# Kernel tuning notes

Hardware: AMD Instinct MI355X
Metric: run time of the kernel (lower is better)

The kernel has to match this reference:

```python
import jax, jax.numpy as jnp
import numpy as np

SOS_TOKEN = 0
MAX_SEQ_LENGTH = 64
H = 1024   # hidden_size
V = 32000  # output_size (vocab)
B = 64     # batch


def setup_inputs() -> dict:
    key = jax.random.key(0)
    ks = jax.random.split(key, 10)
    s = 1.0 / np.sqrt(H)
    return {
        "encoder_outputs": jax.random.normal(ks[0], (B, 32, H), dtype=jnp.float32),
        "encoder_hidden": jax.random.normal(ks[1], (1, B, H), dtype=jnp.float32),
        "target_tensor": jax.random.randint(ks[2], (B, MAX_SEQ_LENGTH), 0, V),
        "emb": jax.random.normal(ks[3], (V, H), dtype=jnp.float32) * 0.02,
        "W_ih": jax.random.uniform(ks[4], (3 * H, H), minval=-s, maxval=s, dtype=jnp.float32),
        "W_hh": jax.random.uniform(ks[5], (3 * H, H), minval=-s, maxval=s, dtype=jnp.float32),
        "b_ih": jax.random.uniform(ks[6], (3 * H,), minval=-s, maxval=s, dtype=jnp.float32),
        "b_hh": jax.random.uniform(ks[7], (3 * H,), minval=-s, maxval=s, dtype=jnp.float32),
        "W_out": jax.random.uniform(ks[8], (V, H), minval=-s, maxval=s, dtype=jnp.float32),
        "b_out": jax.random.uniform(ks[9], (V,), minval=-s, maxval=s, dtype=jnp.float32),
    }


def reference(encoder_outputs, encoder_hidden, target_tensor,
              emb, W_ih, W_hh, b_ih, b_hh, W_out, b_out):
    # teacher forcing: input at step 0 is SOS, at step i>0 is target[:, i-1]
    bsz = encoder_outputs.shape[0]
    sos = jnp.full((bsz, 1), SOS_TOKEN, dtype=target_tensor.dtype)
    tokens = jnp.concatenate([sos, target_tensor[:, :MAX_SEQ_LENGTH - 1]], axis=1).T  # [T,B]
    h0 = encoder_hidden[0]  # num_layers=1 -> [B,H]

    def step(h, tok):
        x = jax.nn.relu(emb[tok])                       # [B,H] embed + relu
        gi = x @ W_ih.T + b_ih                          # [B,3H]
        gh = h @ W_hh.T + b_hh                          # [B,3H]
        ir, iz, inn = jnp.split(gi, 3, axis=-1)         # PyTorch gate order r,z,n
        hr, hz, hn = jnp.split(gh, 3, axis=-1)
        r = jax.nn.sigmoid(ir + hr)
        z = jax.nn.sigmoid(iz + hz)
        n = jnp.tanh(inn + r * hn)
        h_new = (1.0 - z) * n + z * h
        logits = h_new @ W_out.T + b_out                # [B,V]
        return h_new, logits

    h_final, logits = jax.lax.scan(step, h0, tokens)    # logits: [T,B,V]
    dec_out = jax.nn.log_softmax(jnp.transpose(logits, (1, 0, 2)), axis=-1)  # [B,T,V]
    return dec_out, h_final[None]  # hidden: [num_layers,B,H]
```

## Files before the change

### kernel.cpp

```cpp
#include <hip/hip_runtime.h>
#include <hip/hip_bf16.h>
#include <stdint.h>

#define H 1024
#define BATCH 64
#define TSTEPS 64
#define VOCAB 32000

typedef __attribute__((ext_vector_type(8))) short bf16x8;
typedef __attribute__((ext_vector_type(4))) float f32x4;

__device__ __forceinline__ uint16_t f2b(float f) {
  union { float f; uint32_t u; } v; v.f = f;
  uint32_t u = v.u;
  return (uint16_t)((u + 0x7FFFu + ((u >> 16) & 1u)) >> 16);
}

__device__ __forceinline__ void g2l16(const uint16_t* g, uint16_t* l) {
  __builtin_amdgcn_global_load_lds((const __attribute__((address_space(1))) void*)(g),
                                   (__attribute__((address_space(3))) void*)(l), 16, 0, 0);
}

__global__ void cast_bf16_kernel(const float* __restrict__ src, uint16_t* __restrict__ dst, int n4) {
  int i = blockIdx.x * blockDim.x + threadIdx.x;
  int stride = gridDim.x * blockDim.x;
  for (; i < n4; i += stride) {
    float4 f = ((const float4*)src)[i];
    union { uint16_t u[4]; uint64_t d; } o;
    o.u[0] = f2b(f.x); o.u[1] = f2b(f.y); o.u[2] = f2b(f.z); o.u[3] = f2b(f.w);
    ((uint64_t*)dst)[i] = o.d;
  }
}

__global__ void embed_kernel(const float* __restrict__ emb, const int* __restrict__ tgt,
                             uint16_t* __restrict__ X) {
  int i = blockIdx.x;
  int t = i >> 6, b = i & 63;
  int tok = (t == 0) ? 0 : tgt[b * TSTEPS + (t - 1)];
  const float4* src = (const float4*)(emb + (size_t)tok * H);
  uint64_t* dst = (uint64_t*)(X + (size_t)i * H);
  int k = threadIdx.x;
  float4 f = src[k];
  union { uint16_t u[4]; uint64_t d; } o;
  o.u[0] = f2b(fmaxf(f.x, 0.f)); o.u[1] = f2b(fmaxf(f.y, 0.f));
  o.u[2] = f2b(fmaxf(f.z, 0.f)); o.u[3] = f2b(fmaxf(f.w, 0.f));
  dst[k] = o.d;
}

__global__ void h0_kernel(const float* __restrict__ eh, uint16_t* __restrict__ hb0) {
  int i = blockIdx.x * blockDim.x + threadIdx.x;
  float4 f = ((const float4*)eh)[i];
  union { uint16_t u[4]; uint64_t d; } o;
  o.u[0] = f2b(f.x); o.u[1] = f2b(f.y); o.u[2] = f2b(f.z); o.u[3] = f2b(f.w);
  ((uint64_t*)hb0)[i] = o.d;
}

__global__ __launch_bounds__(256) void gi_gemm_kernel(
    const uint16_t* __restrict__ A,
    const uint16_t* __restrict__ Bm,
    const float* __restrict__ bias,
    float* __restrict__ out) {
  __shared__ uint16_t lA[128 * 32];
  __shared__ uint16_t lB[128 * 32];
  const int tid = threadIdx.x;
  const int lane = tid & 63;
  const int w = tid >> 6;
  const int wr = w >> 1, wc = w & 1;
  int flat = blockIdx.y * 24 + blockIdx.x;
  int nf = (flat & 7) * 96 + (flat >> 3);
  const int m0 = (nf / 24) * 128;
  const int n0 = (nf % 24) * 128;

  f32x4 acc[4][4];
#pragma unroll
  for (int mi = 0; mi < 4; ++mi)
#pragma unroll
    for (int ni = 0; ni < 4; ++ni) acc[mi][ni] = (f32x4){0, 0, 0, 0};

  const int srow = w * 16 + (lane >> 2);
  const int scol = (lane & 3) * 8;

  for (int k0 = 0; k0 < 1024; k0 += 32) {
    __syncthreads();
    g2l16(A + (size_t)(m0 + srow) * 1024 + k0 + scol,       &lA[w * 512]);
    g2l16(A + (size_t)(m0 + 64 + srow) * 1024 + k0 + scol,  &lA[2048 + w * 512]);
    g2l16(Bm + (size_t)(n0 + srow) * 1024 + k0 + scol,      &lB[w * 512]);
    g2l16(Bm + (size_t)(n0 + 64 + srow) * 1024 + k0 + scol, &lB[2048 + w * 512]);
    __syncthreads();
    bf16x8 a[4], b[4];
#pragma unroll
    for (int mi = 0; mi < 4; ++mi)
      a[mi] = *(const bf16x8*)&lA[(wr * 64 + mi * 16 + (lane & 15)) * 32 + (lane >> 4) * 8];
#pragma unroll
    for (int ni = 0; ni < 4; ++ni)
      b[ni] = *(const bf16x8*)&lB[(wc * 64 + ni * 16 + (lane & 15)) * 32 + (lane >> 4) * 8];
#pragma unroll
    for (int mi = 0; mi < 4; ++mi)
#pragma unroll
      for (int ni = 0; ni < 4; ++ni)
        acc[mi][ni] = __builtin_amdgcn_mfma_f32_16x16x32_bf16(a[mi], b[ni], acc[mi][ni], 0, 0, 0);
  }

#pragma unroll
  for (int ni = 0; ni < 4; ++ni) {
    int v = n0 + wc * 64 + ni * 16 + (lane & 15);
    float bv = bias[v];
#pragma unroll
    for (int mi = 0; mi < 4; ++mi) {
#pragma unroll
      for (int r = 0; r < 4; ++r) {
        int row = m0 + wr * 64 + mi * 16 + (lane >> 4) * 4 + r;
        out[(size_t)row * 3072 + v] = acc[mi][ni][r] + bv;
      }
    }
  }
}

__global__ __launch_bounds__(64) void step_kernel(
    const uint16_t* __restrict__ Whh_b,
    const float* __restrict__ gi,
    const float* __restrict__ b_hh,
    const float* __restrict__ h_cur,
    float* __restrict__ h_nxt,
    uint16_t* __restrict__ Hsb,
    int t) {
  const int lane = threadIdx.x;
  const int l15 = lane & 15, kq = lane >> 4;
  const int rg = blockIdx.x >> 6, cs = blockIdx.x & 63;
  const int m0 = rg * 16, c0 = cs * 16;
  const int c = c0 + l15;

  float gr[4], gz[4], gn[4], hold[4];
#pragma unroll
  for (int r = 0; r < 4; ++r) {
    int m = m0 + kq * 4 + r;
    const float* gp = gi + (size_t)(t * 64 + m) * 3072;
    gr[r] = gp[c]; gz[r] = gp[1024 + c]; gn[r] = gp[2048 + c];
    hold[r] = h_cur[(size_t)m * 1024 + c];
  }

  const uint16_t* ap = Hsb + (size_t)(t * 64 + m0 + l15) * 1024 + kq * 8;
  const uint16_t* br = Whh_b + (size_t)(c) * 1024 + kq * 8;
  const uint16_t* bz = Whh_b + (size_t)(1024 + c) * 1024 + kq * 8;
  const uint16_t* bn = Whh_b + (size_t)(2048 + c) * 1024 + kq * 8;

  f32x4 ar = {0,0,0,0}, az = {0,0,0,0}, an = {0,0,0,0};
#pragma unroll
  for (int kk = 0; kk < 32; ++kk) {
    bf16x8 a = *(const bf16x8*)(ap + kk * 32);
    ar = __builtin_amdgcn_mfma_f32_16x16x32_bf16(a, *(const bf16x8*)(br + kk * 32), ar, 0, 0, 0);
    az = __builtin_amdgcn_mfma_f32_16x16x32_bf16(a, *(const bf16x8*)(bz + kk * 32), az, 0, 0, 0);
    an = __builtin_amdgcn_mfma_f32_16x16x32_bf16(a, *(const bf16x8*)(bn + kk * 32), an, 0, 0, 0);
  }

  float bhr = b_hh[c], bhz = b_hh[1024 + c], bhn = b_hh[2048 + c];
#pragma unroll
  for (int r = 0; r < 4; ++r) {
    int m = m0 + kq * 4 + r;
    float rg_ = 1.f / (1.f + __expf(-(gr[r] + ar[r] + bhr)));
    float zg  = 1.f / (1.f + __expf(-(gz[r] + az[r] + bhz)));
    float ng  = tanhf(gn[r] + rg_ * (an[r] + bhn));
    float hnew = (1.f - zg) * ng + zg * hold[r];
    h_nxt[(size_t)m * 1024 + c] = hnew;
    Hsb[(size_t)((t + 1) * 64 + m) * 1024 + c] = f2b(hnew);
  }
}

__global__ __launch_bounds__(256) void out_gemm_kernel(
    const uint16_t* __restrict__ A,
    const uint16_t* __restrict__ Bm,
    const float* __restrict__ bias,
    float* __restrict__ out,
    float* __restrict__ px) {
  __shared__ uint16_t lA[128 * 32];
  __shared__ uint16_t lB[128 * 32];
  __shared__ float ssum[128][2];
  const int tid = threadIdx.x;
  const int lane = tid & 63;
  const int w = tid >> 6;
  const int wr = w >> 1, wc = w & 1;
  int flat = blockIdx.y * 250 + blockIdx.x;
  int xcd = flat & 7, i = flat >> 3;
  const int m0 = ((xcd << 2) | (i & 3)) * 128;
  const int n0 = (i >> 2) * 128;

  f32x4 acc[4][4];
#pragma unroll
  for (int mi = 0; mi < 4; ++mi)
#pragma unroll
    for (int ni = 0; ni < 4; ++ni) acc[mi][ni] = (f32x4){0, 0, 0, 0};

  const int srow = w * 16 + (lane >> 2);
  const int scol = (lane & 3) * 8;

  for (int k0 = 0; k0 < 1024; k0 += 32) {
    __syncthreads();
    g2l16(A + (size_t)(m0 + srow) * 1024 + k0 + scol,       &lA[w * 512]);
    g2l16(A + (size_t)(m0 + 64 + srow) * 1024 + k0 + scol,  &lA[2048 + w * 512]);
    g2l16(Bm + (size_t)(n0 + srow) * 1024 + k0 + scol,      &lB[w * 512]);
    g2l16(Bm + (size_t)(n0 + 64 + srow) * 1024 + k0 + scol, &lB[2048 + w * 512]);
    __syncthreads();
    bf16x8 a[4], b[4];
#pragma unroll
    for (int mi = 0; mi < 4; ++mi)
      a[mi] = *(const bf16x8*)&lA[(wr * 64 + mi * 16 + (lane & 15)) * 32 + (lane >> 4) * 8];
#pragma unroll
    for (int ni = 0; ni < 4; ++ni)
      b[ni] = *(const bf16x8*)&lB[(wc * 64 + ni * 16 + (lane & 15)) * 32 + (lane >> 4) * 8];
#pragma unroll
    for (int mi = 0; mi < 4; ++mi)
#pragma unroll
      for (int ni = 0; ni < 4; ++ni)
        acc[mi][ni] = __builtin_amdgcn_mfma_f32_16x16x32_bf16(a[mi], b[ni], acc[mi][ni], 0, 0, 0);
  }

  float rsum[4][4];
#pragma unroll
  for (int mi = 0; mi < 4; ++mi)
#pragma unroll
    for (int r = 0; r < 4; ++r) rsum[mi][r] = 0.f;

#pragma unroll
  for (int ni = 0; ni < 4; ++ni) {
    int v = n0 + wc * 64 + ni * 16 + (lane & 15);
    float bv = bias[v];
#pragma unroll
    for (int mi = 0; mi < 4; ++mi) {
#pragma unroll
      for (int r = 0; r < 4; ++r) {
        float x = acc[mi][ni][r] + bv;
        int row = m0 + wr * 64 + mi * 16 + (lane >> 4) * 4 + r;
        size_t off = (size_t)(row & 63) * (TSTEPS * (size_t)VOCAB)
                   + (size_t)(row >> 6) * VOCAB + v;
        __builtin_nontemporal_store(x, &out[off]);
        rsum[mi][r] += __expf(x);
      }
    }
  }
#pragma unroll
  for (int mask = 1; mask < 16; mask <<= 1)
#pragma unroll
    for (int mi = 0; mi < 4; ++mi)
#pragma unroll
      for (int r = 0; r < 4; ++r)
        rsum[mi][r] += __shfl_xor(rsum[mi][r], mask);

  if ((lane & 15) == 0) {
    int kq = lane >> 4;
#pragma unroll
    for (int mi = 0; mi < 4; ++mi)
#pragma unroll
      for (int r = 0; r < 4; ++r)
        ssum[wr * 64 + mi * 16 + kq * 4 + r][wc] = rsum[mi][r];
  }
  __syncthreads();
  if (tid < 128)
    px[(size_t)(m0 + tid) * 256 + (n0 >> 7)] = ssum[tid][0] + ssum[tid][1];
}

__global__ __launch_bounds__(256) void lsefin_kernel(
    const float* __restrict__ px, float* __restrict__ out) {
  const int tid = threadIdx.x;
  const int b = blockIdx.x >> 6, t = blockIdx.x & 63;
  const float* p = px + (size_t)(t * 64 + b) * 256;
  float s = (tid < 250) ? p[tid] : 0.f;
#pragma unroll
  for (int off = 1; off < 64; off <<= 1) s += __shfl_xor(s, off);
  __shared__ float ss[4];
  if ((tid & 63) == 0) ss[tid >> 6] = s;
  __syncthreads();
  float lse = logf(ss[0] + ss[1] + ss[2] + ss[3]);
  float* row = out + (size_t)blockIdx.x * VOCAB;
  for (int i = tid * 4; i < VOCAB; i += 1024) {
    f32x4 x = *(const f32x4*)(row + i);
    x[0] -= lse; x[1] -= lse; x[2] -= lse; x[3] -= lse;
    __builtin_nontemporal_store(x, (f32x4*)(row + i));
  }
}

__global__ void hcopy_kernel(const float* __restrict__ h, float* __restrict__ out) {
  int i = blockIdx.x * blockDim.x + threadIdx.x;
  ((float4*)out)[i] = ((const float4*)h)[i];
}

extern "C" void kernel_launch(void* const* d_in, const int* in_sizes, int n_in,
                              void* d_out, int out_size, void* d_ws, size_t ws_size,
                              hipStream_t stream) {
  const float* enc_hidden = (const float*)d_in[1];
  const int* tgt          = (const int*)d_in[2];
  const float* emb        = (const float*)d_in[3];
  const float* W_ih       = (const float*)d_in[4];
  const float* W_hh       = (const float*)d_in[5];
  const float* b_ih       = (const float*)d_in[6];
  const float* b_hh       = (const float*)d_in[7];
  const float* W_out      = (const float*)d_in[8];
  const float* b_out      = (const float*)d_in[9];
  float* out = (float*)d_out;

  char* ws = (char*)d_ws;
  float*    gi     = (float*)(ws);
  uint16_t* Wout_b = (uint16_t*)(ws);
  uint16_t* Wih_b  = (uint16_t*)(ws + 65536000);
  uint16_t* Whh_b  = (uint16_t*)(ws + 71827456);
  uint16_t* Xb     = (uint16_t*)(ws + 78118912);
  float*    px     = (float*)   (ws + 78118912);
  uint16_t* Hsb    = (uint16_t*)(ws + 86507520);
  float*    hA     = (float*)   (ws + 95027200);
  float*    hB     = (float*)   (ws + 95289344);

  cast_bf16_kernel<<<2048, 256, 0, stream>>>(W_ih, Wih_b, 3072 * 1024 / 4);
  cast_bf16_kernel<<<2048, 256, 0, stream>>>(W_hh, Whh_b, 3072 * 1024 / 4);
  embed_kernel<<<4096, 256, 0, stream>>>(emb, tgt, Xb);
  h0_kernel<<<64, 256, 0, stream>>>(enc_hidden, Hsb);

  dim3 gg(24, 32);
  gi_gemm_kernel<<<gg, 256, 0, stream>>>(Xb, Wih_b, b_ih, gi);

  for (int t = 0; t < TSTEPS; ++t) {
    const float* hc = (t == 0) ? enc_hidden : ((t & 1) ? hA : hB);
    float* hn       = (t & 1) ? hB : hA;
    step_kernel<<<256, 64, 0, stream>>>(Whh_b, gi, b_hh, hc, hn, Hsb, t);
  }

  cast_bf16_kernel<<<2048, 256, 0, stream>>>(W_out, Wout_b, VOCAB * 1024 / 4);

  dim3 g(250, 32);
  out_gemm_kernel<<<g, 256, 0, stream>>>(Hsb + 65536, Wout_b, b_out, out, px);
  lsefin_kernel<<<4096, 256, 0, stream>>>(px, out);
  hcopy_kernel<<<64, 256, 0, stream>>>((TSTEPS & 1) ? hB : hA, out + 131072000ull);
}
```

Measured before the change: 1.102 ms.

## Rewrite output GEMM as 256x256 tiled, double-buffered swizzled LDS pipeline; regroup step blocks

```diff
diff --git a/kernel.cpp b/kernel.cpp
--- a/kernel.cpp
+++ b/kernel.cpp
@@ -116,7 +116,7 @@
   }
 }
 
-__global__ __launch_bounds__(64) void step_kernel(
+__global__ __launch_bounds__(256) void step_kernel(
     const uint16_t* __restrict__ Whh_b,
     const float* __restrict__ gi,
     const float* __restrict__ b_hh,
@@ -124,10 +124,10 @@
     float* __restrict__ h_nxt,
     uint16_t* __restrict__ Hsb,
     int t) {
-  const int lane = threadIdx.x;
+  const int tid = threadIdx.x;
+  const int lane = tid & 63, w = tid >> 6;
   const int l15 = lane & 15, kq = lane >> 4;
-  const int rg = blockIdx.x >> 6, cs = blockIdx.x & 63;
-  const int m0 = rg * 16, c0 = cs * 16;
+  const int m0 = w * 16, c0 = blockIdx.x * 16;
   const int c = c0 + l15;
 
   float gr[4], gz[4], gn[4], hold[4];
@@ -166,70 +166,147 @@
   }
 }
 
-__global__ __launch_bounds__(256) void out_gemm_kernel(
-    const uint16_t* __restrict__ A,
-    const uint16_t* __restrict__ Bm,
+
+__device__ __forceinline__ void stageAH(const uint16_t* __restrict__ G, int grow0, int kt,
+                                        char* lbase, int w, int l) {
+#pragma unroll
+  for (int j = 0; j < 2; ++j) {
+    int c = w * 2 + j;
+    int r = c * 8 + (l >> 3);
+    int scol = ((l & 7) ^ (l >> 3)) * 8;
+    g2l16(G + (size_t)(grow0 + r) * 1024 + kt * 64 + scol, (uint16_t*)(lbase + c * 1024));
+  }
+}
+
+template<int D, int MP, bool RB>
+__device__ __forceinline__ void ph_read(const char* sm, int wr, int wc, int l15, int kq,
+                                        bf16x8 (&afr)[2][2], bf16x8 (&bfr)[4][2]) {
+#pragma unroll
+  for (int m = 0; m < 2; ++m) {
+    const int mi = MP * 2 + m;
+    const int h = mi >> 2;
+    const int r = wr * 64 + (mi & 3) * 16 + l15;
+    const char* base = sm + D * 65536 + h * 16384 + r * 128;
+#pragma unroll
+    for (int ks = 0; ks < 2; ++ks)
+      afr[m][ks] = *(const bf16x8*)(base + ((((ks << 2) + kq) ^ (r & 7)) << 4));
+  }
+  if constexpr (RB) {
+#pragma unroll
+    for (int ni = 0; ni < 4; ++ni) {
+      const int r = (wc & 1) * 64 + ni * 16 + l15;
+      const char* base = sm + D * 65536 + 32768 + (wc >> 1) * 16384 + r * 128;
+#pragma unroll
+      for (int ks = 0; ks < 2; ++ks)
+        bfr[ni][ks] = *(const bf16x8*)(base + ((((ks << 2) + kq) ^ (r & 7)) << 4));
+    }
+  }
+}
+
+template<int MP>
+__device__ __forceinline__ void ph_mma(f32x4 (&acc)[8][4], bf16x8 (&afr)[2][2], bf16x8 (&bfr)[4][2]) {
+  __builtin_amdgcn_s_setprio(1);
+#pragma unroll
+  for (int m = 0; m < 2; ++m)
+#pragma unroll
+    for (int ni = 0; ni < 4; ++ni)
+#pragma unroll
+      for (int ks = 0; ks < 2; ++ks)
+        acc[MP * 2 + m][ni] =
+            __builtin_amdgcn_mfma_f32_16x16x32_bf16(afr[m][ks], bfr[ni][ks], acc[MP * 2 + m][ni], 0, 0, 0);
+  __builtin_amdgcn_s_setprio(0);
+}
+
+#define PHX(D, MP, RB, STG, VM) { \
+  bf16x8 afr[2][2]; \
+  ph_read<D, MP, RB>(sm, wr, wc, l15, kq, afr, bfr); \
+  STG; \
+  __builtin_amdgcn_sched_barrier(0); \
+  if (VM == 1) asm volatile("s_waitcnt vmcnt(6)" ::: "memory"); \
+  if (VM == 2) asm volatile("s_waitcnt vmcnt(0)" ::: "memory"); \
+  __builtin_amdgcn_s_barrier(); \
+  ph_mma<MP>(acc, afr, bfr); \
+  __builtin_amdgcn_s_barrier(); \
+}
+
+__global__ __launch_bounds__(512, 1) void out_gemm_kernel(
+    const uint16_t* __restrict__ Ag,
+    const uint16_t* __restrict__ Bg,
     const float* __restrict__ bias,
     float* __restrict__ out,
     float* __restrict__ px) {
-  __shared__ uint16_t lA[128 * 32];
-  __shared__ uint16_t lB[128 * 32];
-  __shared__ float ssum[128][2];
+  extern __shared__ char sm[];
   const int tid = threadIdx.x;
-  const int lane = tid & 63;
-  const int w = tid >> 6;
-  const int wr = w >> 1, wc = w & 1;
+  const int l = tid & 63, w = tid >> 6;
+  const int l15 = l & 15, kq = l >> 4;
+  const int wr = w >> 2, wc = w & 3;
   int flat = blockIdx.y * 250 + blockIdx.x;
-  int xcd = flat & 7, i = flat >> 3;
-  const int m0 = ((xcd << 2) | (i & 3)) * 128;
-  const int n0 = (i >> 2) * 128;
-
-  f32x4 acc[4][4];
-#pragma unroll
-  for (int mi = 0; mi < 4; ++mi)
+  int xcd = flat & 7, i0 = flat >> 3;
+  const int m0 = ((xcd << 1) | (i0 & 1)) * 256;
+  const int n0 = (i0 >> 1) * 256;
+
+  char* const sA0 = sm;
+  char* const sA1 = sm + 16384;
+  char* const sB0 = sm + 32768;
+  char* const sB1 = sm + 49152;
+  char* const tA0 = sm + 65536;
+  char* const tA1 = sm + 81920;
+  char* const tB0 = sm + 98304;
+  char* const tB1 = sm + 114688;
+
+  f32x4 acc[8][4];
+#pragma unroll
+  for (int mi = 0; mi < 8; ++mi)
 #pragma unroll
     for (int ni = 0; ni < 4; ++ni) acc[mi][ni] = (f32x4){0, 0, 0, 0};
 
-  const int srow = w * 16 + (lane >> 2);
-  const int scol = (lane & 3) * 8;
-
-  for (int k0 = 0; k0 < 1024; k0 += 32) {
-    __syncthreads();
-    g2l16(A + (size_t)(m0 + srow) * 1024 + k0 + scol,       &lA[w * 512]);
-    g2l16(A + (size_t)(m0 + 64 + srow) * 1024 + k0 + scol,  &lA[2048 + w * 512]);
-    g2l16(Bm + (size_t)(n0 + srow) * 1024 + k0 + scol,      &lB[w * 512]);
-    g2l16(Bm + (size_t)(n0 + 64 + srow) * 1024 + k0 + scol, &lB[2048 + w * 512]);
-    __syncthreads();
-    bf16x8 a[4], b[4];
-#pragma unroll
-    for (int mi = 0; mi < 4; ++mi)
-      a[mi] = *(const bf16x8*)&lA[(wr * 64 + mi * 16 + (lane & 15)) * 32 + (lane >> 4) * 8];
-#pragma unroll
-    for (int ni = 0; ni < 4; ++ni)
-      b[ni] = *(const bf16x8*)&lB[(wc * 64 + ni * 16 + (lane & 15)) * 32 + (lane >> 4) * 8];
-#pragma unroll
-    for (int mi = 0; mi < 4; ++mi)
-#pragma unroll
-      for (int ni = 0; ni < 4; ++ni)
-        acc[mi][ni] = __builtin_amdgcn_mfma_f32_16x16x32_bf16(a[mi], b[ni], acc[mi][ni], 0, 0, 0);
-  }
-
-  float rsum[4][4];
-#pragma unroll
-  for (int mi = 0; mi < 4; ++mi)
+  stageAH(Bg, n0,       0, sB0, w, l);
+  stageAH(Bg, n0 + 128, 0, sB1, w, l);
+  stageAH(Ag, m0,       0, sA0, w, l);
+  stageAH(Ag, m0 + 128, 0, sA1, w, l);
+  stageAH(Bg, n0,       1, tB0, w, l);
+  stageAH(Bg, n0 + 128, 1, tB1, w, l);
+  stageAH(Ag, m0,       1, tA0, w, l);
+  asm volatile("s_waitcnt vmcnt(6)" ::: "memory");
+  __builtin_amdgcn_s_barrier();
+
+  bf16x8 bfr[4][2];
+  for (int i = 0; i < 7; ++i) {
+    PHX(0, 0, true,  stageAH(Ag, m0 + 128, 2 * i + 1, tA1, w, l), 0)
+    PHX(0, 1, false, stageAH(Bg, n0,       2 * i + 2, sB0, w, l), 0)
+    PHX(0, 2, false, stageAH(Bg, n0 + 128, 2 * i + 2, sB1, w, l), 0)
+    PHX(0, 3, false, stageAH(Ag, m0,       2 * i + 2, sA0, w, l), 1)
+    PHX(1, 0, true,  stageAH(Ag, m0 + 128, 2 * i + 2, sA1, w, l), 0)
+    PHX(1, 1, false, stageAH(Bg, n0,       2 * i + 3, tB0, w, l), 0)
+    PHX(1, 2, false, stageAH(Bg, n0 + 128, 2 * i + 3, tB1, w, l), 0)
+    PHX(1, 3, false, stageAH(Ag, m0,       2 * i + 3, tA0, w, l), 1)
+  }
+  PHX(0, 0, true,  stageAH(Ag, m0 + 128, 15, tA1, w, l), 0)
+  PHX(0, 1, false, , 0)
+  PHX(0, 2, false, , 0)
+  PHX(0, 3, false, , 2)
+  PHX(1, 0, true,  , 0)
+  PHX(1, 1, false, , 0)
+  PHX(1, 2, false, , 0)
+  PHX(1, 3, false, , 0)
+
+  float rsum[8][4];
+#pragma unroll
+  for (int mi = 0; mi < 8; ++mi)
 #pragma unroll
     for (int r = 0; r < 4; ++r) rsum[mi][r] = 0.f;
 
 #pragma unroll
   for (int ni = 0; ni < 4; ++ni) {
-    int v = n0 + wc * 64 + ni * 16 + (lane & 15);
+    int v = n0 + wc * 64 + ni * 16 + l15;
     float bv = bias[v];
 #pragma unroll
-    for (int mi = 0; mi < 4; ++mi) {
+    for (int mi = 0; mi < 8; ++mi) {
+      int tr = (mi < 4) ? (wr * 64 + mi * 16) : (128 + wr * 64 + (mi - 4) * 16);
 #pragma unroll
       for (int r = 0; r < 4; ++r) {
         float x = acc[mi][ni][r] + bv;
-        int row = m0 + wr * 64 + mi * 16 + (lane >> 4) * 4 + r;
+        int row = m0 + tr + kq * 4 + r;
         size_t off = (size_t)(row & 63) * (TSTEPS * (size_t)VOCAB)
                    + (size_t)(row >> 6) * VOCAB + v;
         __builtin_nontemporal_store(x, &out[off]);
@@ -240,30 +317,35 @@
 #pragma unroll
   for (int mask = 1; mask < 16; mask <<= 1)
 #pragma unroll
-    for (int mi = 0; mi < 4; ++mi)
+    for (int mi = 0; mi < 8; ++mi)
 #pragma unroll
       for (int r = 0; r < 4; ++r)
         rsum[mi][r] += __shfl_xor(rsum[mi][r], mask);
 
-  if ((lane & 15) == 0) {
-    int kq = lane >> 4;
-#pragma unroll
-    for (int mi = 0; mi < 4; ++mi)
+  __builtin_amdgcn_s_barrier();
+  float* ssum = (float*)sm;
+  if (l15 == 0) {
+#pragma unroll
+    for (int mi = 0; mi < 8; ++mi) {
+      int tr = (mi < 4) ? (wr * 64 + mi * 16) : (128 + wr * 64 + (mi - 4) * 16);
 #pragma unroll
       for (int r = 0; r < 4; ++r)
-        ssum[wr * 64 + mi * 16 + kq * 4 + r][wc] = rsum[mi][r];
-  }
-  __syncthreads();
-  if (tid < 128)
-    px[(size_t)(m0 + tid) * 256 + (n0 >> 7)] = ssum[tid][0] + ssum[tid][1];
+        ssum[(tr + kq * 4 + r) * 4 + wc] = rsum[mi][r];
+    }
+  }
+  __builtin_amdgcn_s_barrier();
+  if (tid < 256) {
+    float t4 = ssum[tid * 4] + ssum[tid * 4 + 1] + ssum[tid * 4 + 2] + ssum[tid * 4 + 3];
+    px[(size_t)(m0 + tid) * 128 + (n0 >> 8)] = t4;
+  }
 }
 
 __global__ __launch_bounds__(256) void lsefin_kernel(
     const float* __restrict__ px, float* __restrict__ out) {
   const int tid = threadIdx.x;
   const int b = blockIdx.x >> 6, t = blockIdx.x & 63;
-  const float* p = px + (size_t)(t * 64 + b) * 256;
-  float s = (tid < 250) ? p[tid] : 0.f;
+  const float* p = px + (size_t)(t * 64 + b) * 128;
+  float s = (tid < 125) ? p[tid] : 0.f;
 #pragma unroll
   for (int off = 1; off < 64; off <<= 1) s += __shfl_xor(s, off);
   __shared__ float ss[4];
@@ -308,6 +390,9 @@
   float*    hA     = (float*)   (ws + 95027200);
   float*    hB     = (float*)   (ws + 95289344);
 
+  hipFuncSetAttribute((const void*)out_gemm_kernel,
+                      hipFuncAttributeMaxDynamicSharedMemorySize, 131072);
+
   cast_bf16_kernel<<<2048, 256, 0, stream>>>(W_ih, Wih_b, 3072 * 1024 / 4);
   cast_bf16_kernel<<<2048, 256, 0, stream>>>(W_hh, Whh_b, 3072 * 1024 / 4);
   embed_kernel<<<4096, 256, 0, stream>>>(emb, tgt, Xb);
@@ -319,13 +404,13 @@
   for (int t = 0; t < TSTEPS; ++t) {
     const float* hc = (t == 0) ? enc_hidden : ((t & 1) ? hA : hB);
     float* hn       = (t & 1) ? hB : hA;
-    step_kernel<<<256, 64, 0, stream>>>(Whh_b, gi, b_hh, hc, hn, Hsb, t);
+    step_kernel<<<64, 256, 0, stream>>>(Whh_b, gi, b_hh, hc, hn, Hsb, t);
   }
 
   cast_bf16_kernel<<<2048, 256, 0, stream>>>(W_out, Wout_b, VOCAB * 1024 / 4);
 
-  dim3 g(250, 32);
-  out_gemm_kernel<<<g, 256, 0, stream>>>(Hsb + 65536, Wout_b, b_out, out, px);
+  dim3 g(250, 8);
+  out_gemm_kernel<<<g, 512, 131072, stream>>>(Hsb + 65536, Wout_b, b_out, out, px);
   lsefin_kernel<<<4096, 256, 0, stream>>>(px, out);
   hcopy_kernel<<<64, 256, 0, stream>>>((TSTEPS & 1) ? hB : hA, out + 131072000ull);
 }
```

Result: slower. 1.641 ms (+48.9%).

## Pipeline output GEMM with double-buffered swizzled LDS and 8-wave blocks

Applied to the files above, without the earlier changes.

```diff
diff --git a/kernel.cpp b/kernel.cpp
--- a/kernel.cpp
+++ b/kernel.cpp
@@ -166,53 +166,112 @@
   }
 }
 
-__global__ __launch_bounds__(256) void out_gemm_kernel(
-    const uint16_t* __restrict__ A,
-    const uint16_t* __restrict__ Bm,
+
+__device__ __forceinline__ void stageAH(const uint16_t* __restrict__ G, int grow0, int kt,
+                                        char* lbase, int w, int l) {
+#pragma unroll
+  for (int j = 0; j < 2; ++j) {
+    int c = w * 2 + j;
+    int r = c * 8 + (l >> 3);
+    int scol = ((l & 7) ^ (l >> 3)) * 8;
+    g2l16(G + (size_t)(grow0 + r) * 1024 + kt * 64 + scol, (uint16_t*)(lbase + c * 1024));
+  }
+}
+
+template<int AOFF, int BOFF, int MPH, bool RB>
+__device__ __forceinline__ void ph_read(const char* sm, int wr, int wc, int l15, int kq,
+                                        bf16x8 (&afr)[2][2], bf16x8 (&bfr)[2][2]) {
+#pragma unroll
+  for (int m = 0; m < 2; ++m) {
+    const int mi = MPH * 2 + m;
+    const int r = wr * 64 + mi * 16 + l15;
+    const char* base = sm + AOFF + r * 128;
+#pragma unroll
+    for (int ks = 0; ks < 2; ++ks)
+      afr[m][ks] = *(const bf16x8*)(base + ((((ks << 2) + kq) ^ (r & 7)) << 4));
+  }
+  if constexpr (RB) {
+#pragma unroll
+    for (int ni = 0; ni < 2; ++ni) {
+      const int r = wc * 32 + ni * 16 + l15;
+      const char* base = sm + BOFF + r * 128;
+#pragma unroll
+      for (int ks = 0; ks < 2; ++ks)
+        bfr[ni][ks] = *(const bf16x8*)(base + ((((ks << 2) + kq) ^ (r & 7)) << 4));
+    }
+  }
+}
+
+template<int MPH>
+__device__ __forceinline__ void ph_mma(f32x4 (&acc)[4][2], bf16x8 (&afr)[2][2], bf16x8 (&bfr)[2][2]) {
+  __builtin_amdgcn_s_setprio(1);
+#pragma unroll
+  for (int m = 0; m < 2; ++m)
+#pragma unroll
+    for (int ni = 0; ni < 2; ++ni)
+#pragma unroll
+      for (int ks = 0; ks < 2; ++ks)
+        acc[MPH * 2 + m][ni] =
+            __builtin_amdgcn_mfma_f32_16x16x32_bf16(afr[m][ks], bfr[ni][ks], acc[MPH * 2 + m][ni], 0, 0, 0);
+  __builtin_amdgcn_s_setprio(0);
+}
+
+#define PH(AOFF, BOFF, MPH, RB, STG, VM) { \
+  bf16x8 afr[2][2]; \
+  ph_read<AOFF, BOFF, MPH, RB>(sm, wr, wc, l15, kq, afr, bfr); \
+  STG; \
+  __builtin_amdgcn_sched_barrier(0); \
+  if (VM == 1) asm volatile("s_waitcnt vmcnt(2)" ::: "memory"); \
+  if (VM == 2) asm volatile("s_waitcnt vmcnt(0)" ::: "memory"); \
+  __builtin_amdgcn_s_barrier(); \
+  ph_mma<MPH>(acc, afr, bfr); \
+  __builtin_amdgcn_s_barrier(); \
+}
+
+__global__ __launch_bounds__(512, 4) void out_gemm_kernel(
+    const uint16_t* __restrict__ Ag,
+    const uint16_t* __restrict__ Bg,
     const float* __restrict__ bias,
     float* __restrict__ out,
     float* __restrict__ px) {
-  __shared__ uint16_t lA[128 * 32];
-  __shared__ uint16_t lB[128 * 32];
-  __shared__ float ssum[128][2];
+  extern __shared__ char sm[];
   const int tid = threadIdx.x;
-  const int lane = tid & 63;
-  const int w = tid >> 6;
-  const int wr = w >> 1, wc = w & 1;
-  int flat = blockIdx.y * 250 + blockIdx.x;
-  int xcd = flat & 7, i = flat >> 3;
-  const int m0 = ((xcd << 2) | (i & 3)) * 128;
-  const int n0 = (i >> 2) * 128;
-
-  f32x4 acc[4][4];
+  const int l = tid & 63, w = tid >> 6;
+  const int l15 = l & 15, kq = l >> 4;
+  const int wr = w >> 2, wc = w & 3;
+  int flat = blockIdx.y * 1000 + blockIdx.x;
+  int xcd = flat & 7, i0 = flat >> 3;
+  const int m0 = ((xcd << 2) | (i0 & 3)) * 128;
+  const int n0 = (i0 >> 2) * 128;
+
+  char* const sA = sm;
+  char* const sB = sm + 16384;
+  char* const tA = sm + 32768;
+  char* const tB = sm + 49152;
+
+  f32x4 acc[4][2];
 #pragma unroll
   for (int mi = 0; mi < 4; ++mi)
 #pragma unroll
-    for (int ni = 0; ni < 4; ++ni) acc[mi][ni] = (f32x4){0, 0, 0, 0};
-
-  const int srow = w * 16 + (lane >> 2);
-  const int scol = (lane & 3) * 8;
-
-  for (int k0 = 0; k0 < 1024; k0 += 32) {
-    __syncthreads();
-    g2l16(A + (size_t)(m0 + srow) * 1024 + k0 + scol,       &lA[w * 512]);
-    g2l16(A + (size_t)(m0 + 64 + srow) * 1024 + k0 + scol,  &lA[2048 + w * 512]);
-    g2l16(Bm + (size_t)(n0 + srow) * 1024 + k0 + scol,      &lB[w * 512]);
-    g2l16(Bm + (size_t)(n0 + 64 + srow) * 1024 + k0 + scol, &lB[2048 + w * 512]);
-    __syncthreads();
-    bf16x8 a[4], b[4];
-#pragma unroll
-    for (int mi = 0; mi < 4; ++mi)
-      a[mi] = *(const bf16x8*)&lA[(wr * 64 + mi * 16 + (lane & 15)) * 32 + (lane >> 4) * 8];
-#pragma unroll
-    for (int ni = 0; ni < 4; ++ni)
-      b[ni] = *(const bf16x8*)&lB[(wc * 64 + ni * 16 + (lane & 15)) * 32 + (lane >> 4) * 8];
-#pragma unroll
-    for (int mi = 0; mi < 4; ++mi)
-#pragma unroll
-      for (int ni = 0; ni < 4; ++ni)
-        acc[mi][ni] = __builtin_amdgcn_mfma_f32_16x16x32_bf16(a[mi], b[ni], acc[mi][ni], 0, 0, 0);
-  }
+    for (int ni = 0; ni < 2; ++ni) acc[mi][ni] = (f32x4){0, 0, 0, 0};
+
+  stageAH(Ag, m0, 0, sA, w, l);
+  stageAH(Bg, n0, 0, sB, w, l);
+  stageAH(Bg, n0, 1, tB, w, l);
+  asm volatile("s_waitcnt vmcnt(2)" ::: "memory");
+  __builtin_amdgcn_s_barrier();
+
+  bf16x8 bfr[2][2];
+  for (int i = 0; i < 7; ++i) {
+    PH(0,     16384, 0, true,  stageAH(Ag, m0, 2 * i + 1, tA, w, l), 0)
+    PH(0,     16384, 1, false, stageAH(Bg, n0, 2 * i + 2, sB, w, l), 1)
+    PH(32768, 49152, 0, true,  stageAH(Ag, m0, 2 * i + 2, sA, w, l), 0)
+    PH(32768, 49152, 1, false, stageAH(Bg, n0, 2 * i + 3, tB, w, l), 1)
+  }
+  PH(0,     16384, 0, true,  stageAH(Ag, m0, 15, tA, w, l), 0)
+  PH(0,     16384, 1, false, , 2)
+  PH(32768, 49152, 0, true,  , 0)
+  PH(32768, 49152, 1, false, , 0)
 
   float rsum[4][4];
 #pragma unroll
@@ -221,15 +280,15 @@
     for (int r = 0; r < 4; ++r) rsum[mi][r] = 0.f;
 
 #pragma unroll
-  for (int ni = 0; ni < 4; ++ni) {
-    int v = n0 + wc * 64 + ni * 16 + (lane & 15);
+  for (int ni = 0; ni < 2; ++ni) {
+    int v = n0 + wc * 32 + ni * 16 + l15;
     float bv = bias[v];
 #pragma unroll
     for (int mi = 0; mi < 4; ++mi) {
 #pragma unroll
       for (int r = 0; r < 4; ++r) {
         float x = acc[mi][ni][r] + bv;
-        int row = m0 + wr * 64 + mi * 16 + (lane >> 4) * 4 + r;
+        int row = m0 + wr * 64 + mi * 16 + kq * 4 + r;
         size_t off = (size_t)(row & 63) * (TSTEPS * (size_t)VOCAB)
                    + (size_t)(row >> 6) * VOCAB + v;
         __builtin_nontemporal_store(x, &out[off]);
@@ -245,17 +304,20 @@
       for (int r = 0; r < 4; ++r)
         rsum[mi][r] += __shfl_xor(rsum[mi][r], mask);
 
-  if ((lane & 15) == 0) {
-    int kq = lane >> 4;
+  float* ssum = (float*)(sm + 65536);
+  __builtin_amdgcn_s_barrier();
+  if (l15 == 0) {
 #pragma unroll
     for (int mi = 0; mi < 4; ++mi)
 #pragma unroll
       for (int r = 0; r < 4; ++r)
-        ssum[wr * 64 + mi * 16 + kq * 4 + r][wc] = rsum[mi][r];
-  }
-  __syncthreads();
-  if (tid < 128)
-    px[(size_t)(m0 + tid) * 256 + (n0 >> 7)] = ssum[tid][0] + ssum[tid][1];
+        ssum[(wr * 64 + mi * 16 + kq * 4 + r) * 4 + wc] = rsum[mi][r];
+  }
+  __builtin_amdgcn_s_barrier();
+  if (tid < 128) {
+    float t4 = ssum[tid * 4] + ssum[tid * 4 + 1] + ssum[tid * 4 + 2] + ssum[tid * 4 + 3];
+    px[(size_t)(m0 + tid) * 256 + (n0 >> 7)] = t4;
+  }
 }
 
 __global__ __launch_bounds__(256) void lsefin_kernel(
@@ -272,7 +334,7 @@
   float lse = logf(ss[0] + ss[1] + ss[2] + ss[3]);
   float* row = out + (size_t)blockIdx.x * VOCAB;
   for (int i = tid * 4; i < VOCAB; i += 1024) {
-    f32x4 x = *(const f32x4*)(row + i);
+    f32x4 x = __builtin_nontemporal_load((const f32x4*)(row + i));
     x[0] -= lse; x[1] -= lse; x[2] -= lse; x[3] -= lse;
     __builtin_nontemporal_store(x, (f32x4*)(row + i));
   }
@@ -308,6 +370,9 @@
   float*    hA     = (float*)   (ws + 95027200);
   float*    hB     = (float*)   (ws + 95289344);
 
+  hipFuncSetAttribute((const void*)out_gemm_kernel,
+                      hipFuncAttributeMaxDynamicSharedMemorySize, 67584);
+
   cast_bf16_kernel<<<2048, 256, 0, stream>>>(W_ih, Wih_b, 3072 * 1024 / 4);
   cast_bf16_kernel<<<2048, 256, 0, stream>>>(W_hh, Whh_b, 3072 * 1024 / 4);
   embed_kernel<<<4096, 256, 0, stream>>>(emb, tgt, Xb);
@@ -324,8 +389,8 @@
 
   cast_bf16_kernel<<<2048, 256, 0, stream>>>(W_out, Wout_b, VOCAB * 1024 / 4);
 
-  dim3 g(250, 32);
-  out_gemm_kernel<<<g, 256, 0, stream>>>(Hsb + 65536, Wout_b, b_out, out, px);
+  dim3 g(1000, 8);
+  out_gemm_kernel<<<g, 512, 67584, stream>>>(Hsb + 65536, Wout_b, b_out, out, px);
   lsefin_kernel<<<4096, 256, 0, stream>>>(px, out);
   hcopy_kernel<<<64, 256, 0, stream>>>((TSTEPS & 1) ? hB : hA, out + 131072000ull);
 }
```

After: 1.023 ms. 1.08x faster.
